# Performance work log

Hardware: AMD Instinct MI355X
Metric: run time of the kernel (lower is better)

## Reference

```python
import jax, jax.numpy as jnp
import numpy as np

N = 2060          # drug-graph nodes (m_drug_d_num)
F_OUT = 901       # out_feats, forced by Linear(901*2, ...)
M = 901 + (N - 1183)  # 1778 fused node rows
E = N * 64
N_TRAIN, N_TEST = 100000, 30000
EPS = 1e-5


def setup_inputs() -> dict:
    key = jax.random.key(0)
    ks = jax.random.split(key, 30)
    f32 = jnp.float32
    inp = {
        'x_feat': jax.random.normal(ks[0], (N, N), f32),
        'mirna_feat': jax.random.normal(ks[1], (M, F_OUT), f32),
        'Wg': jax.random.normal(ks[2], (N, F_OUT), f32) * 0.02,
        'att_src': jax.random.normal(ks[3], (F_OUT,), f32) * 0.05,
        'att_dst': jax.random.normal(ks[4], (F_OUT,), f32) * 0.05,
        'gat_b': jnp.zeros((F_OUT,), f32),
        'lw1': jax.random.normal(ks[5], (1, 2), f32) * 0.5,
        'lb1': jnp.zeros((1,), f32),
        'lw2': jax.random.normal(ks[6], (2, 1), f32) * 0.5,
        'lb2': jnp.zeros((2,), f32),
        'gw1': jax.random.normal(ks[7], (1, 2), f32) * 0.5,
        'gb1': jnp.zeros((1,), f32),
        'gw2': jax.random.normal(ks[8], (2, 1), f32) * 0.5,
        'gb2': jnp.zeros((2,), f32),
        'W1': jax.random.normal(ks[9], (2 * F_OUT, 1024), f32) * 0.02,
        'b1': jnp.zeros((1024,), f32),
        'W2': jax.random.normal(ks[10], (1024, 512), f32) * 0.03,
        'b2': jnp.zeros((512,), f32),
        'W3': jax.random.normal(ks[11], (512, 64), f32) * 0.04,
        'b3': jnp.zeros((64,), f32),
        'W4': jax.random.normal(ks[12], (64, 1), f32) * 0.1,
        'b4': jnp.zeros((1,), f32),
        'edge_index': jax.random.randint(ks[13], (2, E), 0, N, jnp.int32),
        'train_sample': jax.random.randint(ks[14], (N_TRAIN, 2), 0, M, jnp.int32),
        'test_sample': jax.random.randint(ks[15], (N_TEST, 2), 0, M, jnp.int32),
    }
    return inp


def _bn(x, axes):
    # BatchNorm in train mode (fresh module: gamma=1, beta=0, biased batch var)
    mu = x.mean(axes, keepdims=True)
    var = x.var(axes, keepdims=True)
    return (x - mu) * jax.lax.rsqrt(var + EPS)


def _gat(x, Wg, att_src, att_dst, gat_b, edge_index):
    # single-head PyG-style GATConv with self loops, negative_slope=0.2
    h = x @ Wg                                         # [N, F]
    loop = jnp.arange(N, dtype=edge_index.dtype)
    src = jnp.concatenate([edge_index[0], loop])
    dst = jnp.concatenate([edge_index[1], loop])
    a_s = h @ att_src                                  # [N]
    a_d = h @ att_dst
    e = jax.nn.leaky_relu(a_s[src] + a_d[dst], 0.2)    # per-edge logits
    emax = jax.ops.segment_max(e, dst, num_segments=N)
    ex = jnp.exp(e - emax[dst])
    denom = jax.ops.segment_sum(ex, dst, num_segments=N)
    alpha = ex / denom[dst]
    out = jax.ops.segment_sum(alpha[:, None] * h[src], dst, num_segments=N) + gat_b
    return jax.nn.relu(out)                            # F.relu in MGL (MGC relu is idempotent)


def _forward(x_feat, mirna_feat, Wg, att_src, att_dst, gat_b,
             lw1, lb1, lw2, lb2, gw1, gb1, gw2, gb2,
             W1, b1, W2, b2, W3, b3, W4, b4,
             edge_index, train_sample, test_sample):
    g = _gat(x_feat, Wg, att_src, att_dst, gat_b, edge_index)      # [N, 901]
    drug_view = jnp.concatenate([g[:901], g[1183:]], axis=0)       # [M, 901]
    x = jnp.stack([drug_view, mirna_feat], axis=1)                 # [M, 2, 901]  (B=M, C=2, H=1 dropped, W=901)

    # MS_CAM (channels=2, r=2), BN in train mode
    xl = jnp.einsum('mcw,oc->mow', x, lw1) + lb1[None, :, None]    # [M, 1, 901]
    xl = jax.nn.relu(_bn(xl, (0, 2)))
    xl = jnp.einsum('mcw,oc->mow', xl, lw2) + lb2[None, :, None]   # [M, 2, 901]
    xl = _bn(xl, (0, 2))

    gp = x.mean(axis=2)                                            # [M, 2] global avg pool
    xg = gp @ gw1.T + gb1                                          # [M, 1]
    xg = jax.nn.relu(_bn(xg, (0,)))
    xg = xg @ gw2.T + gb2                                          # [M, 2]
    xg = _bn(xg, (0,))

    wei = jax.nn.sigmoid(xl + xg[:, :, None])
    x = x * wei                                                    # [M, 2, 901]
    fused = (x[:, 0, :] + x[:, 1, :]) * 0.5                        # [M, 901]

    def score(pairs):
        emb = jnp.concatenate([fused[pairs[:, 0]], fused[pairs[:, 1]]], axis=1)  # [B, 1802]
        h = emb @ W1 + b1
        h = h @ W2 + b2
        h = h @ W3 + b3
        return jax.nn.sigmoid(h @ W4 + b4)

    return score(train_sample), score(test_sample)


def reference(x_feat, mirna_feat, Wg, att_src, att_dst, gat_b,
              lw1, lb1, lw2, lb2, gw1, gb1, gw2, gb2,
              W1, b1, W2, b2, W3, b3, W4, b4,
              edge_index, train_sample, test_sample):
    return _forward(x_feat, mirna_feat, Wg, att_src, att_dst, gat_b,
                    lw1, lb1, lw2, lb2, gw1, gb1, gw2, gb2,
                    W1, b1, W2, b2, W3, b3, W4, b4,
                    edge_index, train_sample, test_sample)
```

## Files before the change

kernel.cpp:

```cpp
#include <hip/hip_runtime.h>

typedef unsigned short u16;
typedef unsigned int   u32;

#define NN   2060
#define FF   901
#define HP   904
#define MM   1778
#define EE   131840
#define ETOT 133900
#define NTR  100000
#define NOUT 130000
#define MP   2112
#define KP   2080
#define NP   960
#define EPSV 1e-5f
#define NTOT 1601978.0

typedef __attribute__((ext_vector_type(4))) float f32x4;
typedef __attribute__((ext_vector_type(8))) short bf16x8;

#define GLL16(g,l) __builtin_amdgcn_global_load_lds( \
    (const __attribute__((address_space(1))) u32*)(g), \
    (__attribute__((address_space(3))) u32*)(l), 16, 0, 0)

__device__ __forceinline__ float bf2f(u16 u){ return __uint_as_float(((u32)u)<<16); }
__device__ __forceinline__ u16 f2bf(float f){
  u32 b = __float_as_uint(f);
  return (u16)((b + 0x7fffu + ((b>>16)&1u)) >> 16);
}
__device__ __forceinline__ float ldf(const void* p, size_t i, int bf){
  return bf ? bf2f(((const u16*)p)[i]) : ((const float*)p)[i];
}
__device__ __forceinline__ u16 ldb(const void* p, size_t i, int bf){
  return bf ? ((const u16*)p)[i] : f2bf(((const float*)p)[i]);
}
__device__ __forceinline__ float waveSum(float v){
  #pragma unroll
  for (int o = 32; o; o >>= 1) v += __shfl_down(v, o);
  return v;
}
__device__ __forceinline__ int waveSumI(int v){
  #pragma unroll
  for (int o = 32; o; o >>= 1) v += __shfl_down(v, o);
  return v;
}
__device__ __forceinline__ int flagWave(const u32* __restrict__ x){
  int l = threadIdx.x & 63;
  u32 w0 = x[l], w1 = x[l + 64];
  int big = (((w0 >> 7)  & 0xFFu) >= 0xC0u) + (((w0 >> 23) & 0xFFu) >= 0xC0u)
          + (((w1 >> 7)  & 0xFFu) >= 0xC0u) + (((w1 >> 23) & 0xFFu) >= 0xC0u);
  big = waveSumI(big);
  return (__shfl(big, 0) >= 8) ? 0 : 1;
}

__global__ __launch_bounds__(256) void pad_k(const void* __restrict__ X, const void* __restrict__ Wg,
                                             const void* __restrict__ W3, const void* __restrict__ W4,
                                             const void* __restrict__ b3, const void* __restrict__ b4,
                                             u16* __restrict__ Ap, u16* __restrict__ BT,
                                             float* __restrict__ u3, float* __restrict__ cp,
                                             u32* __restrict__ emax, int* __restrict__ cnts,
                                             int* __restrict__ fill, float* __restrict__ denom,
                                             int* bfp){
  __shared__ u16 tt[32][33];
  int bf = flagWave((const u32*)X);
  int bx = blockIdx.x, by = blockIdx.y, tid = threadIdx.x;
  if (bx == 0 && by == 0 && tid == 0) *bfp = bf;
  if (by < MP){
    int col = bx * 256 + tid, row = by;
    if (col >= KP) return;
    u16 v = 0;
    if (row < NN && col < NN) v = ldb(X, (size_t)row * NN + col, bf);
    Ap[(size_t)row * KP + col] = v;
  } else if (by < MP + 1950){
    if (bx) return;
    int t = by - MP;
    int kb = (t % 65) * 32, nb = (t / 65) * 32;
    int tx = tid & 31, ty = tid >> 5;
    #pragma unroll
    for (int i = 0; i < 4; ++i){
      int k = kb + ty + 8*i, n = nb + tx;
      u16 v = 0;
      if (k < NN && n < FF) v = ldb(Wg, (size_t)k * FF + n, bf);
      tt[ty + 8*i][tx] = v;
    }
    __syncthreads();
    #pragma unroll
    for (int i = 0; i < 4; ++i){
      int n = nb + ty + 8*i, k = kb + tx;
      if (n < NP && k < KP) BT[(size_t)n * KP + k] = tt[tx][ty + 8*i];
    }
  } else if (by == MP + 1950){
    if (bx) return;
    for (int i = tid; i < NN; i += 256){ emax[i] = 0u; cnts[i] = 0; fill[i] = 0; denom[i] = 0.f; }
  } else {
    if (bx || tid >= 64) return;
    int ob = by - (MP + 1951);
    float s = (ob < 512) ? ldf(W3, (size_t)ob*64 + tid, bf) * ldf(W4, tid, bf)
                         : ldf(b3, tid, bf) * ldf(W4, tid, bf);
    s = waveSum(s);
    if (tid == 0){ if (ob < 512) u3[ob] = s; else cp[0] = s + ldf(b4, 0, bf); }
  }
}

__global__ __launch_bounds__(256) void gemm_k(const u16* __restrict__ A, const u16* __restrict__ BT,
                                              u16* __restrict__ h){
  __shared__ __align__(16) u16 sA[64*32];
  __shared__ __align__(16) u16 sB[64*32];
  int bm = blockIdx.x * 64, bn = blockIdx.y * 64;
  int tid = threadIdx.x, lane = tid & 63, wave = tid >> 6;
  int wm = (wave >> 1) * 32, wn = (wave & 1) * 32;
  f32x4 acc[2][2] = {};
  int srow = tid >> 2;
  int schunk = (tid & 3) ^ ((tid >> 3) & 3);
  const u16* gA = A  + (size_t)(bm + srow) * KP + schunk * 8;
  const u16* gB = BT + (size_t)(bn + srow) * KP + schunk * 8;
  u16* lA = sA + wave * 512;
  u16* lB = sB + wave * 512;
  int fr = lane & 15, quad = lane >> 4;
  int qs = quad ^ ((fr >> 1) & 3);
  const u16* pa0 = &sA[(wm      + fr) * 32 + qs * 8];
  const u16* pa1 = &sA[(wm + 16 + fr) * 32 + qs * 8];
  const u16* pb0 = &sB[(wn      + fr) * 32 + qs * 8];
  const u16* pb1 = &sB[(wn + 16 + fr) * 32 + qs * 8];
  const int KIT = KP / 32;
  for (int kt = 0; kt < KIT; ++kt){
    __syncthreads();
    GLL16(gA + kt * 32, lA);
    GLL16(gB + kt * 32, lB);
    __syncthreads();
    bf16x8 a0 = *(const bf16x8*)pa0;
    bf16x8 a1 = *(const bf16x8*)pa1;
    bf16x8 b0 = *(const bf16x8*)pb0;
    bf16x8 b1 = *(const bf16x8*)pb1;
    acc[0][0] = __builtin_amdgcn_mfma_f32_16x16x32_bf16(a0, b0, acc[0][0], 0,0,0);
    acc[0][1] = __builtin_amdgcn_mfma_f32_16x16x32_bf16(a0, b1, acc[0][1], 0,0,0);
    acc[1][0] = __builtin_amdgcn_mfma_f32_16x16x32_bf16(a1, b0, acc[1][0], 0,0,0);
    acc[1][1] = __builtin_amdgcn_mfma_f32_16x16x32_bf16(a1, b1, acc[1][1], 0,0,0);
  }
  #pragma unroll
  for (int im = 0; im < 2; ++im)
    #pragma unroll
    for (int in = 0; in < 2; ++in)
      #pragma unroll
      for (int i = 0; i < 4; ++i){
        int row = bm + wm + im*16 + quad*4 + i;
        int col = bn + wn + in*16 + fr;
        if (row < NN && col < FF) h[(size_t)row * HP + col] = f2bf(acc[im][in][i]);
      }
}

__global__ __launch_bounds__(256) void coll2_k(const void* __restrict__ W2, const void* __restrict__ b2,
                                               const float* __restrict__ u3, float* __restrict__ u2,
                                               float* __restrict__ cp, const int* bfp){
  int bf = *bfp;
  int ob = blockIdx.x, tid = threadIdx.x;
  float s = 0;
  if (ob < 1024){
    for (int j = tid; j < 512; j += 256) s += ldf(W2, (size_t)ob * 512 + j, bf) * u3[j];
  } else {
    for (int j = tid; j < 512; j += 256) s += ldf(b2, j, bf) * u3[j];
  }
  s = waveSum(s);
  __shared__ float sh[4];
  if ((tid & 63) == 0) sh[tid>>6] = s;
  __syncthreads();
  if (tid == 0){
    float t = sh[0]+sh[1]+sh[2]+sh[3];
    if (ob < 1024) u2[ob] = t; else cp[1] = t;
  }
}

__global__ __launch_bounds__(64) void asd_k(const u16* __restrict__ h, const void* att_s, const void* att_d,
                                            float* a_s, float* a_d, const int* bfp){
  int bf = *bfp;
  int n = blockIdx.x, tid = threadIdx.x;
  float ss = 0, sd = 0;
  for (int f = tid; f < FF; f += 64){
    float hv = bf2f(h[(size_t)n * HP + f]);
    ss += hv * ldf(att_s, f, bf);
    sd += hv * ldf(att_d, f, bf);
  }
  ss = waveSum(ss); sd = waveSum(sd);
  if (tid == 0){ a_s[n] = ss; a_d[n] = sd; }
}

__global__ __launch_bounds__(256) void edge1_k(const int* __restrict__ ei, const float* __restrict__ a_s,
                                               const float* __restrict__ a_d,
                                               u32* __restrict__ emax, int* __restrict__ counts,
                                               const void* __restrict__ W1, const void* __restrict__ b1,
                                               const float* __restrict__ u2, float* __restrict__ u1,
                                               float* __restrict__ cp, const int* bfp){
  int blk = blockIdx.x, tid = threadIdx.x, bf = *bfp;
  int e = blk * 256 + tid;
  if (e < ETOT){
    int src, dst;
    if (e < EE){ src = ei[e]; dst = ei[EE + e]; } else { src = dst = e - EE; }
    float x = a_s[src] + a_d[dst];
    float ev = x > 0.f ? x : 0.2f * x;
    u32 bits = __float_as_uint(ev);
    u32 enc = (bits & 0x80000000u) ? ~bits : (bits | 0x80000000u);
    atomicMax(&emax[dst], enc);
    atomicAdd(&counts[dst], 1);
  }
  if (blk < 451){
    __shared__ float sh[4];
    #pragma unroll 1
    for (int r = 0; r < 4; ++r){
      int ob = blk * 4 + r;
      if (ob <= 1802){
        float s = 0;
        if (ob < 1802){ for (int j = tid; j < 1024; j += 256) s += ldf(W1, (size_t)ob*1024 + j, bf) * u2[j]; }
        else          { for (int j = tid; j < 1024; j += 256) s += ldf(b1, j, bf) * u2[j]; }
        s = waveSum(s);
        __syncthreads();
        if ((tid & 63) == 0) sh[tid >> 6] = s;
        __syncthreads();
        if (tid == 0){ float t = sh[0]+sh[1]+sh[2]+sh[3]; if (ob < 1802) u1[ob] = t; else cp[2] = t; }
      }
    }
  }
}

__global__ __launch_bounds__(256) void scan_k(const int* __restrict__ counts, int* __restrict__ offs){
  __shared__ int part[256];
  int tid = threadIdx.x;
  const int CH = (NN + 255) / 256;
  int base = tid * CH, s = 0;
  for (int i = 0; i < CH; ++i){ int idx = base + i; if (idx < NN) s += counts[idx]; }
  part[tid] = s;
  __syncthreads();
  if (tid == 0){ int run = 0; for (int i = 0; i < 256; ++i){ int v = part[i]; part[i] = run; run += v; } }
  __syncthreads();
  int run = part[tid];
  for (int i = 0; i < CH; ++i){ int idx = base + i; if (idx < NN){ offs[idx] = run; run += counts[idx]; } }
  if (tid == 255) offs[NN] = run;
}

__global__ __launch_bounds__(256) void edge2_k(const int* __restrict__ ei, const float* __restrict__ a_s,
                                               const float* __restrict__ a_d,
                                               const u32* __restrict__ emax, float* __restrict__ denom,
                                               const int* __restrict__ offs, int* __restrict__ fill,
                                               int* __restrict__ csr_src, float* __restrict__ csr_w){
  int e = blockIdx.x * 256 + threadIdx.x;
  if (e >= ETOT) return;
  int src, dst;
  if (e < EE){ src = ei[e]; dst = ei[EE + e]; } else { src = dst = e - EE; }
  float x = a_s[src] + a_d[dst];
  float ev = x > 0.f ? x : 0.2f * x;
  u32 enc = emax[dst];
  u32 bits = (enc & 0x80000000u) ? (enc & 0x7fffffffu) : ~enc;
  float ex = expf(ev - __uint_as_float(bits));
  atomicAdd(&denom[dst], ex);
  int pos = offs[dst] + atomicAdd(&fill[dst], 1);
  csr_src[pos] = src; csr_w[pos] = ex;
}

__device__ __forceinline__ void acc8(float* a, uint4 v, float w){
  u32 arr[4] = {v.x, v.y, v.z, v.w};
  #pragma unroll
  for (int i = 0; i < 4; ++i){
    a[2*i]   += w * __uint_as_float((arr[i] & 0xFFFFu) << 16);
    a[2*i+1] += w * __uint_as_float(arr[i] & 0xFFFF0000u);
  }
}
__global__ __launch_bounds__(128) void aggr_k(const u16* __restrict__ h, const int* __restrict__ offs,
                                              const int* __restrict__ csr_src, const float* __restrict__ csr_w,
                                              const float* __restrict__ denom, const void* gat_b,
                                              const void* __restrict__ mirna,
                                              const void* lw1, const void* lb1,
                                              float* __restrict__ g, float* __restrict__ gp,
                                              float2* __restrict__ pA, const int* bfp){
  int bf = *bfp;
  int m = blockIdx.x, tid = threadIdx.x;
  int dst = m < 901 ? m : m + 282;
  int o0 = offs[dst], o1 = offs[dst + 1];
  float inv = 1.0f / denom[dst];
  __shared__ int   sS[128];
  __shared__ float sW[128];
  __shared__ float red[4][2];
  const int c = tid;
  float a[8] = {0,0,0,0,0,0,0,0};
  for (int base = o0; base < o1; base += 128){
    int nb = min(128, o1 - base);
    __syncthreads();
    if (tid < nb){ sS[tid] = csr_src[base + tid]; sW[tid] = csr_w[base + tid] * inv; }
    __syncthreads();
    if (c < 113){
      int k = 0;
      for (; k + 4 <= nb; k += 4){
        int   i0 = sS[k], i1 = sS[k+1], i2 = sS[k+2], i3 = sS[k+3];
        float w0 = sW[k], w1 = sW[k+1], w2 = sW[k+2], w3 = sW[k+3];
        uint4 v0 = ((const uint4*)(h + (size_t)i0 * HP))[c];
        uint4 v1 = ((const uint4*)(h + (size_t)i1 * HP))[c];
        uint4 v2 = ((const uint4*)(h + (size_t)i2 * HP))[c];
        uint4 v3 = ((const uint4*)(h + (size_t)i3 * HP))[c];
        acc8(a, v0, w0); acc8(a, v1, w1); acc8(a, v2, w2); acc8(a, v3, w3);
      }
      for (; k < nb; ++k){
        uint4 v0 = ((const uint4*)(h + (size_t)sS[k] * HP))[c];
        acc8(a, v0, sW[k]);
      }
    }
  }
  float w00 = ldf(lw1,0,bf), w01 = ldf(lw1,1,bf), bb = ldf(lb1,0,bf);
  float sx0 = 0, sx1 = 0, sl = 0, sl2 = 0;
  if (c < 113){
    int f0 = 8 * c;
    float r[8];
    #pragma unroll
    for (int i = 0; i < 8; ++i){
      bool inb = (f0 + i) < FF;
      float v = a[i] + (inb ? ldf(gat_b, f0 + i, bf) : 0.f);
      v = v > 0.f ? v : 0.f;
      r[i] = inb ? v : 0.f;
      if (inb){
        float x1 = ldf(mirna, (size_t)m * FF + f0 + i, bf);
        float xl = w00*r[i] + w01*x1 + bb;
        sx0 += r[i]; sx1 += x1; sl += xl; sl2 += xl*xl;
      }
    }
    float4* go = (float4*)(g + (size_t)dst * HP);
    go[2*c]   = make_float4(r[0], r[1], r[2], r[3]);
    go[2*c+1] = make_float4(r[4], r[5], r[6], r[7]);
  }
  sx0 = waveSum(sx0); sx1 = waveSum(sx1); sl = waveSum(sl); sl2 = waveSum(sl2);
  int wv = tid >> 6;
  if ((tid & 63) == 0){ red[0][wv]=sx0; red[1][wv]=sx1; red[2][wv]=sl; red[3][wv]=sl2; }
  __syncthreads();
  if (tid == 0){
    gp[2*m]   = (red[0][0]+red[0][1]) / (float)FF;
    gp[2*m+1] = (red[1][0]+red[1][1]) / (float)FF;
    pA[m] = make_float2(red[2][0]+red[2][1], red[3][0]+red[3][1]);
  }
}

__global__ __launch_bounds__(256) void xg_k(const float* __restrict__ gp, const void* gw1, const void* gb1,
                                            const void* gw2, float* __restrict__ xg2b,
                                            const float2* __restrict__ pA, double* __restrict__ Sd,
                                            const int* bfp){
  int bf = *bfp;
  __shared__ float xs[MM];
  __shared__ float red[2][4];
  __shared__ float bc[3];
  int tid = threadIdx.x;
  float s = 0, s2 = 0;
  for (int m = tid; m < MM; m += 256){ float2 p = pA[m]; s += p.x; s2 += p.y; }
  s = waveSum(s); s2 = waveSum(s2);
  if ((tid & 63) == 0){ red[0][tid>>6] = s; red[1][tid>>6] = s2; }
  __syncthreads();
  if (tid == 0){
    Sd[0] = (double)(red[0][0]+red[0][1]+red[0][2]+red[0][3]);
    Sd[1] = (double)(red[1][0]+red[1][1]+red[1][2]+red[1][3]);
  }
  __syncthreads();
  float g10 = ldf(gw1,0,bf), g11 = ldf(gw1,1,bf), b1v = ldf(gb1,0,bf);
  s = 0; s2 = 0;
  for (int m = tid; m < MM; m += 256){
    float v = g10*gp[2*m] + g11*gp[2*m+1] + b1v;
    xs[m] = v; s += v; s2 += v*v;
  }
  s = waveSum(s); s2 = waveSum(s2);
  __syncthreads();
  if ((tid & 63) == 0){ red[0][tid>>6] = s; red[1][tid>>6] = s2; }
  __syncthreads();
  if (tid == 0){
    float t  = red[0][0]+red[0][1]+red[0][2]+red[0][3];
    float t2 = red[1][0]+red[1][1]+red[1][2]+red[1][3];
    float mean = t / (float)MM, var = t2 / (float)MM - mean*mean;
    bc[0] = mean; bc[1] = rsqrtf(var + EPSV);
  }
  __syncthreads();
  float mean = bc[0], rs = bc[1];
  s = 0; s2 = 0;
  for (int m = tid; m < MM; m += 256){
    float r = (xs[m] - mean) * rs; r = r > 0.f ? r : 0.f;
    xs[m] = r; s += r; s2 += r*r;
  }
  s = waveSum(s); s2 = waveSum(s2);
  __syncthreads();
  if ((tid & 63) == 0){ red[0][tid>>6] = s; red[1][tid>>6] = s2; }
  __syncthreads();
  if (tid == 0){
    float t  = red[0][0]+red[0][1]+red[0][2]+red[0][3];
    float t2 = red[1][0]+red[1][1]+red[1][2]+red[1][3];
    float mrg = t / (float)MM, vrg = t2 / (float)MM - mrg*mrg;
    float g20 = ldf(gw2,0,bf), g21 = ldf(gw2,1,bf);
    bc[0] = mrg;
    bc[1] = g20 * rsqrtf(g20*g20*vrg + EPSV);
    bc[2] = g21 * rsqrtf(g21*g21*vrg + EPSV);
  }
  __syncthreads();
  float mrg = bc[0], c0 = bc[1], c1 = bc[2];
  for (int m = tid; m < MM; m += 256){
    float d = xs[m] - mrg;
    xg2b[2*m] = c0 * d; xg2b[2*m+1] = c1 * d;
  }
}

__global__ __launch_bounds__(256) void statsB_k(const float* __restrict__ g, const void* __restrict__ mirna,
                                                const void* lw1, const void* lb1,
                                                const double* __restrict__ S, float2* __restrict__ pB,
                                                const int* bfp){
  int bf = *bfp;
  int m = blockIdx.x, tid = threadIdx.x;
  int gr = m < 901 ? m : m + 282;
  float w00 = ldf(lw1,0,bf), w01 = ldf(lw1,1,bf), bb = ldf(lb1,0,bf);
  float mu1 = (float)(S[0] / NTOT);
  float rs1 = rsqrtf((float)(S[1] / NTOT) - mu1*mu1 + EPSV);
  float sr = 0, sr2 = 0;
  for (int w = tid; w < FF; w += 256){
    float x0 = g[(size_t)gr * HP + w];
    float x1 = ldf(mirna, (size_t)m * FF + w, bf);
    float xl = w00*x0 + w01*x1 + bb;
    float r = (xl - mu1) * rs1; r = r > 0.f ? r : 0.f;
    sr += r; sr2 += r*r;
  }
  sr = waveSum(sr); sr2 = waveSum(sr2);
  __shared__ float sh[2][4];
  if ((tid & 63) == 0){ sh[0][tid>>6] = sr; sh[1][tid>>6] = sr2; }
  __syncthreads();
  if (tid == 0) pB[m] = make_float2(sh[0][0]+sh[0][1]+sh[0][2]+sh[0][3],
                                    sh[1][0]+sh[1][1]+sh[1][2]+sh[1][3]);
}

__global__ __launch_bounds__(256) void redB_k(const float2* __restrict__ pB, double* __restrict__ Sd){
  int tid = threadIdx.x;
  float s = 0, s2 = 0;
  for (int m = tid; m < MM; m += 256){ float2 p = pB[m]; s += p.x; s2 += p.y; }
  s = waveSum(s); s2 = waveSum(s2);
  __shared__ float sh[2][4];
  if ((tid & 63) == 0){ sh[0][tid>>6] = s; sh[1][tid>>6] = s2; }
  __syncthreads();
  if (tid == 0){
    Sd[2] = (double)(sh[0][0]+sh[0][1]+sh[0][2]+sh[0][3]);
    Sd[3] = (double)(sh[1][0]+sh[1][1]+sh[1][2]+sh[1][3]);
  }
}

__global__ __launch_bounds__(256) void fs_k(const float* __restrict__ g, const void* __restrict__ mirna,
                                            const void* lw1, const void* lb1, const void* lw2,
                                            const double* __restrict__ S, const float* __restrict__ xg2b,
                                            const float* __restrict__ u1,
                                            float* __restrict__ s0, float* __restrict__ s1, const int* bfp){
  int bf = *bfp;
  int m = blockIdx.x, tid = threadIdx.x;
  int gr = m < 901 ? m : m + 282;
  float w00 = ldf(lw1,0,bf), w01 = ldf(lw1,1,bf), bb = ldf(lb1,0,bf);
  float mu1 = (float)(S[0] / NTOT);
  float rs1 = rsqrtf((float)(S[1] / NTOT) - mu1*mu1 + EPSV);
  float mr  = (float)(S[2] / NTOT);
  float vr  = (float)(S[3] / NTOT) - mr*mr;
  float l20 = ldf(lw2,0,bf), l21 = ldf(lw2,1,bf);
  float A0 = l20 * rsqrtf(l20*l20*vr + EPSV);
  float A1 = l21 * rsqrtf(l21*l21*vr + EPSV);
  float xa = xg2b[2*m], xb = xg2b[2*m+1];
  float p0 = 0, p1 = 0;
  for (int w = tid; w < FF; w += 256){
    float x0 = g[(size_t)gr * HP + w];
    float x1 = ldf(mirna, (size_t)m * FF + w, bf);
    float xl = w00*x0 + w01*x1 + bb;
    float r = (xl - mu1) * rs1; r = r > 0.f ? r : 0.f;
    float rc = r - mr;
    float z0 = A0*rc + xa, z1 = A1*rc + xb;
    float sg0 = 1.f / (1.f + expf(-z0));
    float sg1 = 1.f / (1.f + expf(-z1));
    float f = 0.5f * (x0*sg0 + x1*sg1);
    p0 += f * u1[w]; p1 += f * u1[901 + w];
  }
  p0 = waveSum(p0); p1 = waveSum(p1);
  __shared__ float sh[2][4];
  if ((tid & 63) == 0){ sh[0][tid>>6] = p0; sh[1][tid>>6] = p1; }
  __syncthreads();
  if (tid == 0){
    s0[m] = sh[0][0]+sh[0][1]+sh[0][2]+sh[0][3];
    s1[m] = sh[1][0]+sh[1][1]+sh[1][2]+sh[1][3];
  }
}

__global__ __launch_bounds__(256) void out_k(const int* __restrict__ tr, const int* __restrict__ te,
                                             const float* __restrict__ s0, const float* __restrict__ s1,
                                             const float* __restrict__ cp, void* __restrict__ out,
                                             const int* bfp){
  int bf = *bfp;
  int b = blockIdx.x * 256 + threadIdx.x;
  if (b >= NOUT) return;
  int i, j;
  if (b < NTR){ i = tr[2*b]; j = tr[2*b + 1]; }
  else { int t = b - NTR; i = te[2*t]; j = te[2*t + 1]; }
  float z = s0[i] + s1[j] + cp[0] + cp[1] + cp[2];
  float v = 1.f / (1.f + expf(-z));
  if (bf) ((u16*)out)[b] = f2bf(v);
  else    ((float*)out)[b] = v;
}

extern "C" void kernel_launch(void* const* d_in, const int* in_sizes, int n_in,
                              void* d_out, int out_size, void* d_ws, size_t ws_size,
                              hipStream_t stream){
  const void* x_feat = d_in[0];
  const void* mirna  = d_in[1];
  const void* Wg     = d_in[2];
  const void* att_s  = d_in[3];
  const void* att_d  = d_in[4];
  const void* gat_b  = d_in[5];
  const void* lw1    = d_in[6];
  const void* lb1    = d_in[7];
  const void* lw2    = d_in[8];
  const void* gw1    = d_in[10];
  const void* gb1    = d_in[11];
  const void* gw2    = d_in[12];
  const void* W1     = d_in[14];
  const void* b1     = d_in[15];
  const void* W2     = d_in[16];
  const void* b2     = d_in[17];
  const void* W3     = d_in[18];
  const void* b3     = d_in[19];
  const void* W4     = d_in[20];
  const void* b4     = d_in[21];
  const int* ei      = (const int*)d_in[22];
  const int* tr      = (const int*)d_in[23];
  const int* te      = (const int*)d_in[24];

  char* ws = (char*)d_ws;
  size_t off = 0;
  auto alloc = [&](size_t bytes)->size_t{ size_t o = off; off += (bytes + 255) & ~(size_t)255; return o; };
  size_t oA  = alloc((size_t)MP*KP*2);
  size_t oBT = alloc((size_t)NP*KP*2);
  size_t oH  = alloc((size_t)NN*HP*2);
  size_t oCS = alloc((size_t)ETOT*4);
  size_t oCW = alloc((size_t)ETOT*4);
  size_t oAS = alloc(NN*4);
  size_t oAD = alloc(NN*4);
  size_t oOF = alloc((NN+1)*4);
  size_t oGP = alloc(MM*2*4);
  size_t oXG = alloc(MM*2*4);
  size_t oS0 = alloc(MM*4);
  size_t oS1 = alloc(MM*4);
  size_t oU3 = alloc(512*4);
  size_t oU2 = alloc(1024*4);
  size_t oU1 = alloc(1802*4);
  size_t oPA = alloc(MM*8);
  size_t oPB = alloc(MM*8);
  size_t oSS = alloc(4*8);
  size_t oCP = alloc(3*4);
  size_t oBF = alloc(4);
  size_t oMX = alloc(NN*4);
  size_t oDN = alloc(NN*4);
  size_t oCT = alloc(NN*4);
  size_t oFL = alloc(NN*4);

  u16*   Ap   = (u16*)(ws+oA);
  u16*   BT   = (u16*)(ws+oBT);
  u16*   h    = (u16*)(ws+oH);
  float* gbuf = (float*)(ws+oA);
  int*   csrS = (int*)(ws+oCS);
  float* csrW = (float*)(ws+oCW);
  float* a_s  = (float*)(ws+oAS);
  float* a_d  = (float*)(ws+oAD);
  int*   offs = (int*)(ws+oOF);
  float* gp   = (float*)(ws+oGP);
  float* xg2b = (float*)(ws+oXG);
  float* s0   = (float*)(ws+oS0);
  float* s1   = (float*)(ws+oS1);
  float* u3   = (float*)(ws+oU3);
  float* u2   = (float*)(ws+oU2);
  float* u1   = (float*)(ws+oU1);
  float2* pA  = (float2*)(ws+oPA);
  float2* pB  = (float2*)(ws+oPB);
  double* Sd  = (double*)(ws+oSS);
  float* cp   = (float*)(ws+oCP);
  int*   bfp  = (int*)(ws+oBF);
  u32*   emax = (u32*)(ws+oMX);
  float* denom= (float*)(ws+oDN);
  int*   cnts = (int*)(ws+oCT);
  int*   fill = (int*)(ws+oFL);

  pad_k  <<<dim3(9, MP + 1950 + 1 + 513), 256, 0, stream>>>(
      x_feat, Wg, W3, W4, b3, b4, Ap, BT, u3, cp, emax, cnts, fill, denom, bfp);
  gemm_k <<<dim3(MP/64, NP/64), 256, 0, stream>>>(Ap, BT, h);
  coll2_k<<<1025, 256, 0, stream>>>(W2, b2, u3, u2, cp, bfp);
  asd_k  <<<NN, 64, 0, stream>>>(h, att_s, att_d, a_s, a_d, bfp);
  edge1_k<<<(ETOT+255)/256, 256, 0, stream>>>(ei, a_s, a_d, emax, cnts, W1, b1, u2, u1, cp, bfp);
  scan_k <<<1, 256, 0, stream>>>(cnts, offs);
  edge2_k<<<(ETOT+255)/256, 256, 0, stream>>>(ei, a_s, a_d, emax, denom, offs, fill, csrS, csrW);
  aggr_k <<<MM, 128, 0, stream>>>(h, offs, csrS, csrW, denom, gat_b, mirna, lw1, lb1, gbuf, gp, pA, bfp);
  xg_k   <<<1, 256, 0, stream>>>(gp, gw1, gb1, gw2, xg2b, pA, Sd, bfp);
  statsB_k<<<MM, 256, 0, stream>>>(gbuf, mirna, lw1, lb1, Sd, pB, bfp);
  redB_k <<<1, 256, 0, stream>>>(pB, Sd);
  fs_k   <<<MM, 256, 0, stream>>>(gbuf, mirna, lw1, lb1, lw2, Sd, xg2b, u1, s0, s1, bfp);
  out_k  <<<(NOUT+255)/256, 256, 0, stream>>>(tr, te, s0, s1, cp, d_out, bfp);
}
```

Baseline: 284.3 us.

## Fuse small kernels, drop softmax max pass, double-buffer GEMM, vectorize padding

Several ideas land together. The edge counting moves into the padding kernel and the W2 collapse merges with the scan, while the W1 collapse now runs as extra blocks of the GEMM kernel. The GAT softmax max-subtraction pass is removed, so exp is applied to raw logits. The GEMM LDS tiles are double-buffered so the next tile loads during the MFMAs, and padding uses 8-wide vector loads with a 1D grid. Together these cut the launch count and serial passes, at the risk of exp overflow for large logits.

```diff
diff --git a/kernel.cpp b/kernel.cpp
--- a/kernel.cpp
+++ b/kernel.cpp
@@ -53,28 +53,48 @@
   big = waveSumI(big);
   return (__shfl(big, 0) >= 8) ? 0 : 1;
 }
+__device__ __forceinline__ void edgeSD(const int* __restrict__ ei, int e, int& src, int& dst){
+  if (e < EE){ src = ei[e]; dst = ei[EE + e]; } else { src = dst = e - EE; }
+}
 
 __global__ __launch_bounds__(256) void pad_k(const void* __restrict__ X, const void* __restrict__ Wg,
                                              const void* __restrict__ W3, const void* __restrict__ W4,
                                              const void* __restrict__ b3, const void* __restrict__ b4,
+                                             const int* __restrict__ ei,
                                              u16* __restrict__ Ap, u16* __restrict__ BT,
                                              float* __restrict__ u3, float* __restrict__ cp,
-                                             u32* __restrict__ emax, int* __restrict__ cnts,
-                                             int* __restrict__ fill, float* __restrict__ denom,
-                                             int* bfp){
+                                             int* __restrict__ cnts, int* bfp){
   __shared__ u16 tt[32][33];
   int bf = flagWave((const u32*)X);
-  int bx = blockIdx.x, by = blockIdx.y, tid = threadIdx.x;
-  if (bx == 0 && by == 0 && tid == 0) *bfp = bf;
-  if (by < MP){
-    int col = bx * 256 + tid, row = by;
-    if (col >= KP) return;
-    u16 v = 0;
-    if (row < NN && col < NN) v = ldb(X, (size_t)row * NN + col, bf);
-    Ap[(size_t)row * KP + col] = v;
-  } else if (by < MP + 1950){
-    if (bx) return;
-    int t = by - MP;
+  int blk = blockIdx.x, tid = threadIdx.x;
+  if (blk == 0 && tid == 0) *bfp = bf;
+  if (blk < MP){
+    int row = blk;
+    for (int c0 = tid * 8; c0 < KP; c0 += 2048){
+      u16 v[8] = {0,0,0,0,0,0,0,0};
+      if (row < NN){
+        if (c0 + 8 <= NN){
+          if (bf){
+            ushort4 t0 = *(const ushort4*)((const u16*)X + (size_t)row * NN + c0);
+            ushort4 t1 = *(const ushort4*)((const u16*)X + (size_t)row * NN + c0 + 4);
+            v[0]=t0.x; v[1]=t0.y; v[2]=t0.z; v[3]=t0.w;
+            v[4]=t1.x; v[5]=t1.y; v[6]=t1.z; v[7]=t1.w;
+          } else {
+            float4 t0 = *(const float4*)((const float*)X + (size_t)row * NN + c0);
+            float4 t1 = *(const float4*)((const float*)X + (size_t)row * NN + c0 + 4);
+            v[0]=f2bf(t0.x); v[1]=f2bf(t0.y); v[2]=f2bf(t0.z); v[3]=f2bf(t0.w);
+            v[4]=f2bf(t1.x); v[5]=f2bf(t1.y); v[6]=f2bf(t1.z); v[7]=f2bf(t1.w);
+          }
+        } else {
+          #pragma unroll
+          for (int i = 0; i < 8; ++i)
+            if (c0 + i < NN) v[i] = ldb(X, (size_t)row * NN + c0 + i, bf);
+        }
+      }
+      *(uint4*)(Ap + (size_t)row * KP + c0) = *(const uint4*)v;
+    }
+  } else if (blk < MP + 1950){
+    int t = blk - MP;
     int kb = (t % 65) * 32, nb = (t / 65) * 32;
     int tx = tid & 31, ty = tid >> 5;
     #pragma unroll
@@ -90,49 +110,110 @@
       int n = nb + ty + 8*i, k = kb + tx;
       if (n < NP && k < KP) BT[(size_t)n * KP + k] = tt[tx][ty + 8*i];
     }
-  } else if (by == MP + 1950){
-    if (bx) return;
-    for (int i = tid; i < NN; i += 256){ emax[i] = 0u; cnts[i] = 0; fill[i] = 0; denom[i] = 0.f; }
-  } else {
-    if (bx || tid >= 64) return;
-    int ob = by - (MP + 1951);
+  } else if (blk < MP + 1950 + 514){
+    if (tid >= 64) return;
+    int ob = blk - (MP + 1950);
+    if (ob > 512) return;
     float s = (ob < 512) ? ldf(W3, (size_t)ob*64 + tid, bf) * ldf(W4, tid, bf)
                          : ldf(b3, tid, bf) * ldf(W4, tid, bf);
     s = waveSum(s);
     if (tid == 0){ if (ob < 512) u3[ob] = s; else cp[0] = s + ldf(b4, 0, bf); }
+  } else {
+    int e = (blk - (MP + 1950 + 514)) * 256 + tid;
+    if (e >= ETOT) return;
+    int src, dst; edgeSD(ei, e, src, dst);
+    atomicAdd(&cnts[dst], 1);
+  }
+}
+
+__global__ __launch_bounds__(256) void scan_k(const int* __restrict__ counts, int* __restrict__ offs,
+                                              const void* __restrict__ W2, const void* __restrict__ b2,
+                                              const float* __restrict__ u3, float* __restrict__ u2,
+                                              float* __restrict__ cp, const int* bfp){
+  int blk = blockIdx.x, tid = threadIdx.x;
+  if (blk == 0){
+    __shared__ int part[256];
+    const int CH = (NN + 255) / 256;
+    int base = tid * CH, s = 0;
+    for (int i = 0; i < CH; ++i){ int idx = base + i; if (idx < NN) s += counts[idx]; }
+    part[tid] = s;
+    __syncthreads();
+    if (tid == 0){ int run = 0; for (int i = 0; i < 256; ++i){ int v = part[i]; part[i] = run; run += v; } }
+    __syncthreads();
+    int run = part[tid];
+    for (int i = 0; i < CH; ++i){ int idx = base + i; if (idx < NN){ offs[idx] = run; run += counts[idx]; } }
+    if (tid == 255) offs[NN] = run;
+  } else {
+    int bf = *bfp;
+    __shared__ float sh[4];
+    #pragma unroll 1
+    for (int r = 0; r < 2; ++r){
+      int ob = (blk - 1) * 2 + r;
+      if (ob <= 1024){
+        float s = 0;
+        if (ob < 1024){ for (int j = tid; j < 512; j += 256) s += ldf(W2, (size_t)ob*512 + j, bf) * u3[j]; }
+        else          { for (int j = tid; j < 512; j += 256) s += ldf(b2, j, bf) * u3[j]; }
+        s = waveSum(s);
+        __syncthreads();
+        if ((tid & 63) == 0) sh[tid >> 6] = s;
+        __syncthreads();
+        if (tid == 0){ float t = sh[0]+sh[1]+sh[2]+sh[3]; if (ob < 1024) u2[ob] = t; else cp[1] = t; }
+      }
+    }
   }
 }
 
 __global__ __launch_bounds__(256) void gemm_k(const u16* __restrict__ A, const u16* __restrict__ BT,
-                                              u16* __restrict__ h){
-  __shared__ __align__(16) u16 sA[64*32];
-  __shared__ __align__(16) u16 sB[64*32];
-  int bm = blockIdx.x * 64, bn = blockIdx.y * 64;
-  int tid = threadIdx.x, lane = tid & 63, wave = tid >> 6;
+                                              u16* __restrict__ h,
+                                              const void* __restrict__ W1, const void* __restrict__ b1,
+                                              const float* __restrict__ u2, float* __restrict__ u1,
+                                              float* __restrict__ cp, const int* bfp){
+  __shared__ __align__(16) u16 sA[2][64*32];
+  __shared__ __align__(16) u16 sB[2][64*32];
+  __shared__ float shr[4];
+  int blk = blockIdx.x, tid = threadIdx.x;
+  if (blk >= 495){
+    int bf = *bfp;
+    #pragma unroll 1
+    for (int r = 0; r < 4; ++r){
+      int ob = (blk - 495) * 4 + r;
+      if (ob <= 1802){
+        float s = 0;
+        if (ob < 1802){ for (int j = tid; j < 1024; j += 256) s += ldf(W1, (size_t)ob*1024 + j, bf) * u2[j]; }
+        else          { for (int j = tid; j < 1024; j += 256) s += ldf(b1, j, bf) * u2[j]; }
+        s = waveSum(s);
+        __syncthreads();
+        if ((tid & 63) == 0) shr[tid >> 6] = s;
+        __syncthreads();
+        if (tid == 0){ float t = shr[0]+shr[1]+shr[2]+shr[3]; if (ob < 1802) u1[ob] = t; else cp[2] = t; }
+      }
+    }
+    return;
+  }
+  int bm = (blk % 33) * 64, bn = (blk / 33) * 64;
+  int lane = tid & 63, wave = tid >> 6;
   int wm = (wave >> 1) * 32, wn = (wave & 1) * 32;
   f32x4 acc[2][2] = {};
   int srow = tid >> 2;
   int schunk = (tid & 3) ^ ((tid >> 3) & 3);
   const u16* gA = A  + (size_t)(bm + srow) * KP + schunk * 8;
   const u16* gB = BT + (size_t)(bn + srow) * KP + schunk * 8;
-  u16* lA = sA + wave * 512;
-  u16* lB = sB + wave * 512;
   int fr = lane & 15, quad = lane >> 4;
   int qs = quad ^ ((fr >> 1) & 3);
-  const u16* pa0 = &sA[(wm      + fr) * 32 + qs * 8];
-  const u16* pa1 = &sA[(wm + 16 + fr) * 32 + qs * 8];
-  const u16* pb0 = &sB[(wn      + fr) * 32 + qs * 8];
-  const u16* pb1 = &sB[(wn + 16 + fr) * 32 + qs * 8];
   const int KIT = KP / 32;
+  GLL16(gA, &sA[0][wave * 512]);
+  GLL16(gB, &sB[0][wave * 512]);
   for (int kt = 0; kt < KIT; ++kt){
+    int cur = kt & 1;
     __syncthreads();
-    GLL16(gA + kt * 32, lA);
-    GLL16(gB + kt * 32, lB);
-    __syncthreads();
-    bf16x8 a0 = *(const bf16x8*)pa0;
-    bf16x8 a1 = *(const bf16x8*)pa1;
-    bf16x8 b0 = *(const bf16x8*)pb0;
-    bf16x8 b1 = *(const bf16x8*)pb1;
+    if (kt + 1 < KIT){
+      GLL16(gA + (kt + 1) * 32, &sA[cur ^ 1][wave * 512]);
+      GLL16(gB + (kt + 1) * 32, &sB[cur ^ 1][wave * 512]);
+    }
+    bf16x8 a0 = *(const bf16x8*)&sA[cur][(wm      + fr) * 32 + qs * 8];
+    bf16x8 a1 = *(const bf16x8*)&sA[cur][(wm + 16 + fr) * 32 + qs * 8];
+    bf16x8 b0 = *(const bf16x8*)&sB[cur][(wn      + fr) * 32 + qs * 8];
+    bf16x8 b1 = *(const bf16x8*)&sB[cur][(wn + 16 + fr) * 32 + qs * 8];
     acc[0][0] = __builtin_amdgcn_mfma_f32_16x16x32_bf16(a0, b0, acc[0][0], 0,0,0);
     acc[0][1] = __builtin_amdgcn_mfma_f32_16x16x32_bf16(a0, b1, acc[0][1], 0,0,0);
     acc[1][0] = __builtin_amdgcn_mfma_f32_16x16x32_bf16(a1, b0, acc[1][0], 0,0,0);
@@ -150,107 +231,32 @@
       }
 }
 
-__global__ __launch_bounds__(256) void coll2_k(const void* __restrict__ W2, const void* __restrict__ b2,
-                                               const float* __restrict__ u3, float* __restrict__ u2,
-                                               float* __restrict__ cp, const int* bfp){
+__global__ __launch_bounds__(256) void asd_k(const u16* __restrict__ h, const void* att_s, const void* att_d,
+                                             float* a_s, float* a_d, const int* bfp){
   int bf = *bfp;
-  int ob = blockIdx.x, tid = threadIdx.x;
-  float s = 0;
-  if (ob < 1024){
-    for (int j = tid; j < 512; j += 256) s += ldf(W2, (size_t)ob * 512 + j, bf) * u3[j];
-  } else {
-    for (int j = tid; j < 512; j += 256) s += ldf(b2, j, bf) * u3[j];
-  }
-  s = waveSum(s);
-  __shared__ float sh[4];
-  if ((tid & 63) == 0) sh[tid>>6] = s;
-  __syncthreads();
-  if (tid == 0){
-    float t = sh[0]+sh[1]+sh[2]+sh[3];
-    if (ob < 1024) u2[ob] = t; else cp[1] = t;
-  }
-}
-
-__global__ __launch_bounds__(64) void asd_k(const u16* __restrict__ h, const void* att_s, const void* att_d,
-                                            float* a_s, float* a_d, const int* bfp){
-  int bf = *bfp;
-  int n = blockIdx.x, tid = threadIdx.x;
+  int wv = threadIdx.x >> 6, lane = threadIdx.x & 63;
+  int n = blockIdx.x * 4 + wv;
+  if (n >= NN) return;
   float ss = 0, sd = 0;
-  for (int f = tid; f < FF; f += 64){
+  for (int f = lane; f < FF; f += 64){
     float hv = bf2f(h[(size_t)n * HP + f]);
     ss += hv * ldf(att_s, f, bf);
     sd += hv * ldf(att_d, f, bf);
   }
   ss = waveSum(ss); sd = waveSum(sd);
-  if (tid == 0){ a_s[n] = ss; a_d[n] = sd; }
-}
-
-__global__ __launch_bounds__(256) void edge1_k(const int* __restrict__ ei, const float* __restrict__ a_s,
-                                               const float* __restrict__ a_d,
-                                               u32* __restrict__ emax, int* __restrict__ counts,
-                                               const void* __restrict__ W1, const void* __restrict__ b1,
-                                               const float* __restrict__ u2, float* __restrict__ u1,
-                                               float* __restrict__ cp, const int* bfp){
-  int blk = blockIdx.x, tid = threadIdx.x, bf = *bfp;
-  int e = blk * 256 + tid;
-  if (e < ETOT){
-    int src, dst;
-    if (e < EE){ src = ei[e]; dst = ei[EE + e]; } else { src = dst = e - EE; }
-    float x = a_s[src] + a_d[dst];
-    float ev = x > 0.f ? x : 0.2f * x;
-    u32 bits = __float_as_uint(ev);
-    u32 enc = (bits & 0x80000000u) ? ~bits : (bits | 0x80000000u);
-    atomicMax(&emax[dst], enc);
-    atomicAdd(&counts[dst], 1);
-  }
-  if (blk < 451){
-    __shared__ float sh[4];
-    #pragma unroll 1
-    for (int r = 0; r < 4; ++r){
-      int ob = blk * 4 + r;
-      if (ob <= 1802){
-        float s = 0;
-        if (ob < 1802){ for (int j = tid; j < 1024; j += 256) s += ldf(W1, (size_t)ob*1024 + j, bf) * u2[j]; }
-        else          { for (int j = tid; j < 1024; j += 256) s += ldf(b1, j, bf) * u2[j]; }
-        s = waveSum(s);
-        __syncthreads();
-        if ((tid & 63) == 0) sh[tid >> 6] = s;
-        __syncthreads();
-        if (tid == 0){ float t = sh[0]+sh[1]+sh[2]+sh[3]; if (ob < 1802) u1[ob] = t; else cp[2] = t; }
-      }
-    }
-  }
-}
-
-__global__ __launch_bounds__(256) void scan_k(const int* __restrict__ counts, int* __restrict__ offs){
-  __shared__ int part[256];
-  int tid = threadIdx.x;
-  const int CH = (NN + 255) / 256;
-  int base = tid * CH, s = 0;
-  for (int i = 0; i < CH; ++i){ int idx = base + i; if (idx < NN) s += counts[idx]; }
-  part[tid] = s;
-  __syncthreads();
-  if (tid == 0){ int run = 0; for (int i = 0; i < 256; ++i){ int v = part[i]; part[i] = run; run += v; } }
-  __syncthreads();
-  int run = part[tid];
-  for (int i = 0; i < CH; ++i){ int idx = base + i; if (idx < NN){ offs[idx] = run; run += counts[idx]; } }
-  if (tid == 255) offs[NN] = run;
+  if (lane == 0){ a_s[n] = ss; a_d[n] = sd; }
 }
 
 __global__ __launch_bounds__(256) void edge2_k(const int* __restrict__ ei, const float* __restrict__ a_s,
-                                               const float* __restrict__ a_d,
-                                               const u32* __restrict__ emax, float* __restrict__ denom,
+                                               const float* __restrict__ a_d, float* __restrict__ denom,
                                                const int* __restrict__ offs, int* __restrict__ fill,
                                                int* __restrict__ csr_src, float* __restrict__ csr_w){
   int e = blockIdx.x * 256 + threadIdx.x;
   if (e >= ETOT) return;
-  int src, dst;
-  if (e < EE){ src = ei[e]; dst = ei[EE + e]; } else { src = dst = e - EE; }
+  int src, dst; edgeSD(ei, e, src, dst);
   float x = a_s[src] + a_d[dst];
   float ev = x > 0.f ? x : 0.2f * x;
-  u32 enc = emax[dst];
-  u32 bits = (enc & 0x80000000u) ? (enc & 0x7fffffffu) : ~enc;
-  float ex = expf(ev - __uint_as_float(bits));
+  float ex = expf(ev);
   atomicAdd(&denom[dst], ex);
   int pos = offs[dst] + atomicAdd(&fill[dst], 1);
   csr_src[pos] = src; csr_w[pos] = ex;
@@ -544,10 +550,11 @@
   size_t oSS = alloc(4*8);
   size_t oCP = alloc(3*4);
   size_t oBF = alloc(4);
-  size_t oMX = alloc(NN*4);
-  size_t oDN = alloc(NN*4);
+  size_t zstart = off;
   size_t oCT = alloc(NN*4);
   size_t oFL = alloc(NN*4);
+  size_t oDN = alloc(NN*4);
+  size_t zend = off;
 
   u16*   Ap   = (u16*)(ws+oA);
   u16*   BT   = (u16*)(ws+oBT);
@@ -570,19 +577,18 @@
   double* Sd  = (double*)(ws+oSS);
   float* cp   = (float*)(ws+oCP);
   int*   bfp  = (int*)(ws+oBF);
-  u32*   emax = (u32*)(ws+oMX);
-  float* denom= (float*)(ws+oDN);
   int*   cnts = (int*)(ws+oCT);
   int*   fill = (int*)(ws+oFL);
-
-  pad_k  <<<dim3(9, MP + 1950 + 1 + 513), 256, 0, stream>>>(
-      x_feat, Wg, W3, W4, b3, b4, Ap, BT, u3, cp, emax, cnts, fill, denom, bfp);
-  gemm_k <<<dim3(MP/64, NP/64), 256, 0, stream>>>(Ap, BT, h);
-  coll2_k<<<1025, 256, 0, stream>>>(W2, b2, u3, u2, cp, bfp);
-  asd_k  <<<NN, 64, 0, stream>>>(h, att_s, att_d, a_s, a_d, bfp);
-  edge1_k<<<(ETOT+255)/256, 256, 0, stream>>>(ei, a_s, a_d, emax, cnts, W1, b1, u2, u1, cp, bfp);
-  scan_k <<<1, 256, 0, stream>>>(cnts, offs);
-  edge2_k<<<(ETOT+255)/256, 256, 0, stream>>>(ei, a_s, a_d, emax, denom, offs, fill, csrS, csrW);
+  float* denom= (float*)(ws+oDN);
+
+  hipMemsetAsync(ws + zstart, 0, zend - zstart, stream);
+
+  pad_k  <<<MP + 1950 + 514 + (ETOT+255)/256, 256, 0, stream>>>(
+      x_feat, Wg, W3, W4, b3, b4, ei, Ap, BT, u3, cp, cnts, bfp);
+  scan_k <<<514, 256, 0, stream>>>(cnts, offs, W2, b2, u3, u2, cp, bfp);
+  gemm_k <<<495 + 451, 256, 0, stream>>>(Ap, BT, h, W1, b1, u2, u1, cp, bfp);
+  asd_k  <<<(NN+3)/4, 256, 0, stream>>>(h, att_s, att_d, a_s, a_d, bfp);
+  edge2_k<<<(ETOT+255)/256, 256, 0, stream>>>(ei, a_s, a_d, denom, offs, fill, csrS, csrW);
   aggr_k <<<MM, 128, 0, stream>>>(h, offs, csrS, csrW, denom, gat_b, mirna, lw1, lb1, gbuf, gp, pA, bfp);
   xg_k   <<<1, 256, 0, stream>>>(gp, gw1, gb1, gw2, xg2b, pA, Sd, bfp);
   statsB_k<<<MM, 256, 0, stream>>>(gbuf, mirna, lw1, lb1, Sd, pB, bfp);
```

Result: faster. 259.4 us (-8.7%).
